# Kernel tuning notes

Hardware: AMD Instinct MI355X
Metric: run time of the kernel (lower is better)

The kernel has to match this reference:

```python
import jax, jax.numpy as jnp
import numpy as np

N = 100000   # nodes
E = 1600000  # edges
IN, HID, OUT = 128, 128, 64

def setup_inputs() -> dict:
    key = jax.random.key(0)
    ks = jax.random.split(key, 18)
    def lin(k, i, o):
        kw, kb = jax.random.split(k)
        s = 1.0 / np.sqrt(i)
        return (jax.random.uniform(kw, (i, o), jnp.float32, -s, s),
                jax.random.uniform(kb, (o,), jnp.float32, -s, s))
    x = jax.random.normal(ks[0], (N, IN), jnp.float32)
    edge_index = jax.random.randint(ks[1], (2, E), 0, N, jnp.int64)
    W1, b1   = lin(ks[2], IN, HID)
    W21, b21 = lin(ks[3], IN, HID)
    W22, b22 = lin(ks[4], HID, HID)
    W31, b31 = lin(ks[5], IN, HID)
    W32, b32 = lin(ks[6], HID, HID)
    W33, b33 = lin(ks[7], HID, HID)
    Wa, ba   = lin(ks[8], HID, 1)
    Wf, bf   = lin(ks[9], HID, OUT)
    return dict(x=x, edge_index=edge_index, W1=W1, b1=b1, W21=W21, b21=b21,
                W22=W22, b22=b22, W31=W31, b31=b31, W32=W32, b32=b32,
                W33=W33, b33=b33, Wa=Wa, ba=ba, Wf=Wf, bf=bf)

def _gcn(x, W, b, src, dst, dinv):
    # PyG GCNConv: D^{-1/2}(A+I)D^{-1/2} X W + b, self-loops added.
    h = x @ W                                    # [N, F]
    norm = dinv[src] * dinv[dst]                 # [E]
    agg = jax.ops.segment_sum(h[src] * norm[:, None], dst, num_segments=N)
    agg = agg + h * (dinv * dinv)[:, None]       # self-loop contribution
    return agg + b

def reference(x, edge_index, W1, b1, W21, b21, W22, b22, W31, b31,
              W32, b32, W33, b33, Wa, ba, Wf, bf):
    src, dst = edge_index[0], edge_index[1]
    # degree with self-loops (in-degree at target nodes)
    deg = jax.ops.segment_sum(jnp.ones(E, x.dtype), dst, num_segments=N) + 1.0
    dinv = jax.lax.rsqrt(deg)
    h1 = jax.nn.relu(_gcn(x, W1, b1, src, dst, dinv))
    h2 = jax.nn.relu(_gcn(x, W21, b21, src, dst, dinv))
    h2 = jax.nn.relu(_gcn(h2, W22, b22, src, dst, dinv))
    h3 = jax.nn.relu(_gcn(x, W31, b31, src, dst, dinv))
    h3 = jax.nn.relu(_gcn(h3, W32, b32, src, dst, dinv))
    h3 = jax.nn.relu(_gcn(h3, W33, b33, src, dst, dinv))
    H = jnp.stack([h1, h2, h3], axis=1)          # [N, 3, HID]
    scores = H @ Wa + ba                         # [N, 3, 1]
    w = jax.nn.softmax(scores, axis=1)
    h_meta = jnp.sum(w * H, axis=1)              # [N, HID]
    h_out = h_meta + h1
    return h_out @ Wf + bf                       # [N, OUT]
```

## Files before the change

kernel.cpp:

```cpp
#include <hip/hip_runtime.h>
#include <hip/hip_bf16.h>

#define HIDF 128
#define OUTF 64
#define SCAN_B 256

__device__ __forceinline__ float us2f(unsigned u_lo16) {
    return __uint_as_float(u_lo16 << 16);
}
__device__ __forceinline__ unsigned short f2us(float f) {
    __hip_bfloat16 h = __float2bfloat16(f);
    return *reinterpret_cast<unsigned short*>(&h);
}
__device__ __forceinline__ unsigned pack2(float a, float b) {
    return (unsigned)f2us(a) | ((unsigned)f2us(b) << 16);
}

__global__ __launch_bounds__(256) void deg_zero(int* __restrict__ d, int N) {
    int i = blockIdx.x * 256 + threadIdx.x;
    if (i < N) d[i] = 0;
}

__global__ __launch_bounds__(256) void deg_count(const int* __restrict__ ei, int* __restrict__ d, int E) {
    int e = blockIdx.x * 256 + threadIdx.x;
    if (e < E) atomicAdd(&d[ei[E + e]], 1);
}

__global__ __launch_bounds__(256) void scanA(const int* __restrict__ degi, int* __restrict__ blocksum, int N) {
    __shared__ int red[256];
    const int b = blockIdx.x;
    const int chunk = (N + SCAN_B - 1) / SCAN_B;
    const int lo = b * chunk, hi = min(lo + chunk, N);
    int s = 0;
    for (int i = lo + threadIdx.x; i < hi; i += 256) s += degi[i];
    red[threadIdx.x] = s;
    __syncthreads();
    for (int off = 128; off; off >>= 1) {
        if (threadIdx.x < off) red[threadIdx.x] += red[threadIdx.x + off];
        __syncthreads();
    }
    if (threadIdx.x == 0) blocksum[b] = red[0];
}

__global__ __launch_bounds__(256) void scanB(const int* __restrict__ blocksum, int* __restrict__ blockoff) {
    __shared__ int ps[256];
    const int t = threadIdx.x;
    ps[t] = blocksum[t];
    __syncthreads();
    for (int off = 1; off < 256; off <<= 1) {
        int v = ps[t];
        int u = (t >= off) ? ps[t - off] : 0;
        __syncthreads();
        ps[t] = v + u;
        __syncthreads();
    }
    blockoff[t] = (t == 0) ? 0 : ps[t - 1];
}

__global__ __launch_bounds__(256) void scanC(const int* __restrict__ degi,
                                             const int* __restrict__ blockoff,
                                             int* __restrict__ cursor,
                                             float* __restrict__ dinv, int N) {
    __shared__ int ps[256];
    const int b = blockIdx.x;
    const int chunk = (N + SCAN_B - 1) / SCAN_B;
    const int lo = b * chunk, hi = min(lo + chunk, N);
    const int tchunk = (chunk + 255) / 256;
    const int tlo = lo + threadIdx.x * tchunk;
    const int thi = min(tlo + tchunk, hi);
    int s = 0;
    for (int i = tlo; i < thi; ++i) s += degi[i];
    ps[threadIdx.x] = s;
    __syncthreads();
    for (int off = 1; off < 256; off <<= 1) {
        int v = ps[threadIdx.x];
        int u = (threadIdx.x >= off) ? ps[threadIdx.x - off] : 0;
        __syncthreads();
        ps[threadIdx.x] = v + u;
        __syncthreads();
    }
    int base = blockoff[b] + ((threadIdx.x == 0) ? 0 : ps[threadIdx.x - 1]);
    for (int i = tlo; i < thi; ++i) {
        int d = degi[i];
        cursor[i] = base;
        base += d;
        dinv[i] = rsqrtf((float)d + 1.f);
    }
}

__global__ __launch_bounds__(256) void scatter_kernel(const int* __restrict__ ei,
                                                      int* __restrict__ cursor,
                                                      int* __restrict__ csr_src, int E) {
    int e = blockIdx.x * 256 + threadIdx.x;
    if (e >= E) return;
    int pos = atomicAdd(&cursor[ei[E + e]], 1);
    csr_src[pos] = ei[e];
}

__global__ __launch_bounds__(256) void cvt_scale(const float* __restrict__ X,
                                                 const float* __restrict__ dinv,
                                                 unsigned short* __restrict__ TB, int N) {
    int g = blockIdx.x * 256 + threadIdx.x;
    if (g >= N * 32) return;
    int n = g >> 5;
    float dv = dinv[n];
    float4 v = ((const float4*)X)[g];
    ushort4 o;
    o.x = f2us(v.x * dv); o.y = f2us(v.y * dv);
    o.z = f2us(v.z * dv); o.w = f2us(v.w * dv);
    ((ushort4*)TB)[g] = o;
}

template <bool OUT_BF16>
__global__ __launch_bounds__(256) void agg_b(const unsigned short* __restrict__ TB,
                                             const float* __restrict__ dinv,
                                             const int* __restrict__ csr_src,
                                             const int* __restrict__ rend,
                                             void* __restrict__ O, int N) {
    const int n = (blockIdx.x * 256 + threadIdx.x) >> 6;
    const int lane = threadIdx.x & 63;
    if (n >= N) return;
    const int start = (n == 0) ? 0 : rend[n - 1];
    const int end   = rend[n];
    const unsigned* Tv = (const unsigned*)TB;

    float ax0 = 0.f, ay0 = 0.f, ax1 = 0.f, ay1 = 0.f;
    int e = start;
    for (; e + 8 <= end; e += 8) {
        int s0 = csr_src[e + 0], s1 = csr_src[e + 1], s2 = csr_src[e + 2], s3 = csr_src[e + 3];
        int s4 = csr_src[e + 4], s5 = csr_src[e + 5], s6 = csr_src[e + 6], s7 = csr_src[e + 7];
        unsigned v0 = Tv[(size_t)s0 * 64 + lane];
        unsigned v1 = Tv[(size_t)s1 * 64 + lane];
        unsigned v2 = Tv[(size_t)s2 * 64 + lane];
        unsigned v3 = Tv[(size_t)s3 * 64 + lane];
        unsigned v4 = Tv[(size_t)s4 * 64 + lane];
        unsigned v5 = Tv[(size_t)s5 * 64 + lane];
        unsigned v6 = Tv[(size_t)s6 * 64 + lane];
        unsigned v7 = Tv[(size_t)s7 * 64 + lane];
        ax0 += us2f(v0 & 0xffffu); ay0 += __uint_as_float(v0 & 0xffff0000u);
        ax1 += us2f(v1 & 0xffffu); ay1 += __uint_as_float(v1 & 0xffff0000u);
        ax0 += us2f(v2 & 0xffffu); ay0 += __uint_as_float(v2 & 0xffff0000u);
        ax1 += us2f(v3 & 0xffffu); ay1 += __uint_as_float(v3 & 0xffff0000u);
        ax0 += us2f(v4 & 0xffffu); ay0 += __uint_as_float(v4 & 0xffff0000u);
        ax1 += us2f(v5 & 0xffffu); ay1 += __uint_as_float(v5 & 0xffff0000u);
        ax0 += us2f(v6 & 0xffffu); ay0 += __uint_as_float(v6 & 0xffff0000u);
        ax1 += us2f(v7 & 0xffffu); ay1 += __uint_as_float(v7 & 0xffff0000u);
    }
    if (e + 4 <= end) {
        int s0 = csr_src[e + 0], s1 = csr_src[e + 1], s2 = csr_src[e + 2], s3 = csr_src[e + 3];
        unsigned v0 = Tv[(size_t)s0 * 64 + lane];
        unsigned v1 = Tv[(size_t)s1 * 64 + lane];
        unsigned v2 = Tv[(size_t)s2 * 64 + lane];
        unsigned v3 = Tv[(size_t)s3 * 64 + lane];
        ax0 += us2f(v0 & 0xffffu); ay0 += __uint_as_float(v0 & 0xffff0000u);
        ax1 += us2f(v1 & 0xffffu); ay1 += __uint_as_float(v1 & 0xffff0000u);
        ax0 += us2f(v2 & 0xffffu); ay0 += __uint_as_float(v2 & 0xffff0000u);
        ax1 += us2f(v3 & 0xffffu); ay1 += __uint_as_float(v3 & 0xffff0000u);
        e += 4;
    }
    for (; e < end; ++e) {
        int s = csr_src[e];
        unsigned v = Tv[(size_t)s * 64 + lane];
        ax0 += us2f(v & 0xffffu);
        ay0 += __uint_as_float(v & 0xffff0000u);
    }
    unsigned sv = Tv[(size_t)n * 64 + lane];
    ax0 += us2f(sv & 0xffffu);
    ay0 += __uint_as_float(sv & 0xffff0000u);
    const float dv = dinv[n];
    float ox = (ax0 + ax1) * dv;
    float oy = (ay0 + ay1) * dv;
    if (OUT_BF16) {
        ((unsigned*)O)[(size_t)n * 64 + lane] = pack2(ox, oy);
    } else {
        float2 o; o.x = ox; o.y = oy;
        ((float2*)O)[(size_t)n * 64 + lane] = o;
    }
}

__global__ __launch_bounds__(256) void agg_dual(const unsigned short* __restrict__ TB23,
                                                const float* __restrict__ dinv,
                                                const int* __restrict__ csr_src,
                                                const int* __restrict__ rend,
                                                unsigned* __restrict__ OA,
                                                unsigned* __restrict__ OB, int N) {
    const int n = (blockIdx.x * 256 + threadIdx.x) >> 6;
    const int lane = threadIdx.x & 63;
    if (n >= N) return;
    const int start = (n == 0) ? 0 : rend[n - 1];
    const int end   = rend[n];
    const unsigned* Tv = (const unsigned*)TB23;

    float ax2 = 0.f, ay2 = 0.f, bx2 = 0.f, by2 = 0.f;
    float ax3 = 0.f, ay3 = 0.f, bx3 = 0.f, by3 = 0.f;
    int e = start;
    for (; e + 4 <= end; e += 4) {
        int s0 = csr_src[e + 0], s1 = csr_src[e + 1], s2 = csr_src[e + 2], s3 = csr_src[e + 3];
        unsigned a0 = Tv[(size_t)s0 * 128 + lane];
        unsigned c0 = Tv[(size_t)s0 * 128 + 64 + lane];
        unsigned a1 = Tv[(size_t)s1 * 128 + lane];
        unsigned c1 = Tv[(size_t)s1 * 128 + 64 + lane];
        unsigned a2 = Tv[(size_t)s2 * 128 + lane];
        unsigned c2 = Tv[(size_t)s2 * 128 + 64 + lane];
        unsigned a3 = Tv[(size_t)s3 * 128 + lane];
        unsigned c3 = Tv[(size_t)s3 * 128 + 64 + lane];
        ax2 += us2f(a0 & 0xffffu); ay2 += __uint_as_float(a0 & 0xffff0000u);
        ax3 += us2f(c0 & 0xffffu); ay3 += __uint_as_float(c0 & 0xffff0000u);
        bx2 += us2f(a1 & 0xffffu); by2 += __uint_as_float(a1 & 0xffff0000u);
        bx3 += us2f(c1 & 0xffffu); by3 += __uint_as_float(c1 & 0xffff0000u);
        ax2 += us2f(a2 & 0xffffu); ay2 += __uint_as_float(a2 & 0xffff0000u);
        ax3 += us2f(c2 & 0xffffu); ay3 += __uint_as_float(c2 & 0xffff0000u);
        bx2 += us2f(a3 & 0xffffu); by2 += __uint_as_float(a3 & 0xffff0000u);
        bx3 += us2f(c3 & 0xffffu); by3 += __uint_as_float(c3 & 0xffff0000u);
    }
    for (; e < end; ++e) {
        int s = csr_src[e];
        unsigned a = Tv[(size_t)s * 128 + lane];
        unsigned c = Tv[(size_t)s * 128 + 64 + lane];
        ax2 += us2f(a & 0xffffu); ay2 += __uint_as_float(a & 0xffff0000u);
        ax3 += us2f(c & 0xffffu); ay3 += __uint_as_float(c & 0xffff0000u);
    }
    {
        unsigned a = Tv[(size_t)n * 128 + lane];
        unsigned c = Tv[(size_t)n * 128 + 64 + lane];
        ax2 += us2f(a & 0xffffu); ay2 += __uint_as_float(a & 0xffff0000u);
        ax3 += us2f(c & 0xffffu); ay3 += __uint_as_float(c & 0xffff0000u);
    }
    const float dv = dinv[n];
    OA[(size_t)n * 64 + lane] = pack2((ax2 + bx2) * dv, (ay2 + by2) * dv);
    OB[(size_t)n * 64 + lane] = pack2((ax3 + bx3) * dv, (ay3 + by3) * dv);
}

#define IM_F32 0
#define IM_BF16 1
#define OM_F32 0
#define OM_BF16 1
#define OM_BF16_SR 2
template <int IMODE, int OMODE>
__global__ __launch_bounds__(256) void gemm128d(const void* __restrict__ Xv,
                                                const float* __restrict__ W,
                                                const float* __restrict__ bias,
                                                const float* __restrict__ dinv,
                                                void* __restrict__ T, int N) {
    __shared__ float Xs[HIDF][68];
    const int tid = threadIdx.x;
    const int nb = blockIdx.x * 64;

    {
        const int nloc = tid & 63;
        const int n = nb + nloc;
        const int kq0 = tid >> 6;
        if (n < N) {
            if (IMODE == IM_F32) {
                const float4* Xr = (const float4*)((const float*)Xv + (size_t)n * HIDF);
                #pragma unroll
                for (int kq = kq0; kq < 32; kq += 4) {
                    float4 v = Xr[kq];
                    int k = kq * 4;
                    Xs[k + 0][nloc] = v.x;
                    Xs[k + 1][nloc] = v.y;
                    Xs[k + 2][nloc] = v.z;
                    Xs[k + 3][nloc] = v.w;
                }
            } else {
                const ushort4* Xr = (const ushort4*)((const unsigned short*)Xv + (size_t)n * HIDF);
                #pragma unroll
                for (int kq = kq0; kq < 32; kq += 4) {
                    ushort4 v = Xr[kq];
                    int k = kq * 4;
                    Xs[k + 0][nloc] = us2f(v.x);
                    Xs[k + 1][nloc] = us2f(v.y);
                    Xs[k + 2][nloc] = us2f(v.z);
                    Xs[k + 3][nloc] = us2f(v.w);
                }
            }
        } else {
            #pragma unroll
            for (int kq = kq0; kq < 32; kq += 4) {
                int k = kq * 4;
                Xs[k + 0][nloc] = 0.f; Xs[k + 1][nloc] = 0.f;
                Xs[k + 2][nloc] = 0.f; Xs[k + 3][nloc] = 0.f;
            }
        }
    }
    __syncthreads();

    const int j4  = tid & 31;
    const int sub = tid >> 5;
    const float4* Wrow = (const float4*)W;
    const float4 bv = ((const float4*)bias)[j4];

    float4 acc[8];
    #pragma unroll
    for (int i = 0; i < 8; ++i) acc[i] = bv;

    #pragma unroll 4
    for (int k = 0; k < HIDF; ++k) {
        float4 w = Wrow[k * 32 + j4];
        float xv[8];
        *(float4*)&xv[0] = *(const float4*)&Xs[k][sub * 8];
        *(float4*)&xv[4] = *(const float4*)&Xs[k][sub * 8 + 4];
        #pragma unroll
        for (int i = 0; i < 8; ++i) {
            acc[i].x = fmaf(xv[i], w.x, acc[i].x);
            acc[i].y = fmaf(xv[i], w.y, acc[i].y);
            acc[i].z = fmaf(xv[i], w.z, acc[i].z);
            acc[i].w = fmaf(xv[i], w.w, acc[i].w);
        }
    }

    #pragma unroll
    for (int i = 0; i < 8; ++i) {
        int n = nb + sub * 8 + i;
        if (n >= N) continue;
        float4 o = acc[i];
        if (OMODE == OM_BF16_SR) {
            float dv = dinv[n];
            o.x = fmaxf(o.x, 0.f) * dv; o.y = fmaxf(o.y, 0.f) * dv;
            o.z = fmaxf(o.z, 0.f) * dv; o.w = fmaxf(o.w, 0.f) * dv;
        }
        if (OMODE == OM_F32) {
            *((float4*)((float*)T + (size_t)n * HIDF + j4 * 4)) = o;
        } else {
            ushort4 u;
            u.x = f2us(o.x); u.y = f2us(o.y); u.z = f2us(o.z); u.w = f2us(o.w);
            *((ushort4*)((unsigned short*)T + (size_t)n * HIDF + j4 * 4)) = u;
        }
    }
}

__global__ __launch_bounds__(256) void gemm_dualA(const float* __restrict__ X,
                                                  const float* __restrict__ W21,
                                                  const float* __restrict__ b21,
                                                  const float* __restrict__ W31,
                                                  const float* __restrict__ b31,
                                                  const float* __restrict__ dinv,
                                                  unsigned short* __restrict__ TB23, int N) {
    __shared__ float Xs[HIDF][68];
    const int tid = threadIdx.x;
    const int nb = blockIdx.x * 64;

    {
        const int nloc = tid & 63;
        const int n = nb + nloc;
        const int kq0 = tid >> 6;
        if (n < N) {
            const float4* Xr = (const float4*)(X + (size_t)n * HIDF);
            #pragma unroll
            for (int kq = kq0; kq < 32; kq += 4) {
                float4 v = Xr[kq];
                int k = kq * 4;
                Xs[k + 0][nloc] = v.x;
                Xs[k + 1][nloc] = v.y;
                Xs[k + 2][nloc] = v.z;
                Xs[k + 3][nloc] = v.w;
            }
        } else {
            #pragma unroll
            for (int kq = kq0; kq < 32; kq += 4) {
                int k = kq * 4;
                Xs[k + 0][nloc] = 0.f; Xs[k + 1][nloc] = 0.f;
                Xs[k + 2][nloc] = 0.f; Xs[k + 3][nloc] = 0.f;
            }
        }
    }
    __syncthreads();

    const int j4  = tid & 31;
    const int sub = tid >> 5;
    const float4* W2r = (const float4*)W21;
    const float4* W3r = (const float4*)W31;
    const float4 bv2 = ((const float4*)b21)[j4];
    const float4 bv3 = ((const float4*)b31)[j4];

    float4 acc2[8], acc3[8];
    #pragma unroll
    for (int i = 0; i < 8; ++i) { acc2[i] = bv2; acc3[i] = bv3; }

    #pragma unroll 2
    for (int k = 0; k < HIDF; ++k) {
        float4 w2 = W2r[k * 32 + j4];
        float4 w3 = W3r[k * 32 + j4];
        float xv[8];
        *(float4*)&xv[0] = *(const float4*)&Xs[k][sub * 8];
        *(float4*)&xv[4] = *(const float4*)&Xs[k][sub * 8 + 4];
        #pragma unroll
        for (int i = 0; i < 8; ++i) {
            acc2[i].x = fmaf(xv[i], w2.x, acc2[i].x);
            acc2[i].y = fmaf(xv[i], w2.y, acc2[i].y);
            acc2[i].z = fmaf(xv[i], w2.z, acc2[i].z);
            acc2[i].w = fmaf(xv[i], w2.w, acc2[i].w);
            acc3[i].x = fmaf(xv[i], w3.x, acc3[i].x);
            acc3[i].y = fmaf(xv[i], w3.y, acc3[i].y);
            acc3[i].z = fmaf(xv[i], w3.z, acc3[i].z);
            acc3[i].w = fmaf(xv[i], w3.w, acc3[i].w);
        }
    }

    #pragma unroll
    for (int i = 0; i < 8; ++i) {
        int n = nb + sub * 8 + i;
        if (n >= N) continue;
        float dv = dinv[n];
        float4 o2 = acc2[i], o3 = acc3[i];
        ushort4 u2, u3;
        u2.x = f2us(fmaxf(o2.x, 0.f) * dv); u2.y = f2us(fmaxf(o2.y, 0.f) * dv);
        u2.z = f2us(fmaxf(o2.z, 0.f) * dv); u2.w = f2us(fmaxf(o2.w, 0.f) * dv);
        u3.x = f2us(fmaxf(o3.x, 0.f) * dv); u3.y = f2us(fmaxf(o3.y, 0.f) * dv);
        u3.z = f2us(fmaxf(o3.z, 0.f) * dv); u3.w = f2us(fmaxf(o3.w, 0.f) * dv);
        unsigned short* base = TB23 + (size_t)n * 256;
        *((ushort4*)(base + j4 * 4)) = u2;
        *((ushort4*)(base + 128 + j4 * 4)) = u3;
    }
}

__global__ __launch_bounds__(256) void meta_kernel(const float* __restrict__ H1,
                                                   const unsigned short* __restrict__ H2B,
                                                   const unsigned short* __restrict__ H3B,
                                                   const float* __restrict__ Wa,
                                                   const float* __restrict__ ba,
                                                   const float* __restrict__ Wf,
                                                   const float* __restrict__ bfb,
                                                   float* __restrict__ out, int N) {
    __shared__ float WfS[HIDF * OUTF];
    __shared__ float WaS[HIDF];
    __shared__ float hm[4][HIDF];
    const int tid = threadIdx.x;
    for (int i = tid; i < HIDF * OUTF; i += 256) WfS[i] = Wf[i];
    if (tid < HIDF) WaS[tid] = Wa[tid];
    __syncthreads();
    const float bav = ba[0];
    const int w = tid >> 6;
    const int l = tid & 63;
    const float bfv = bfb[l];
    const int iters = (N + 3) >> 2;

    for (int it = blockIdx.x; it < iters; it += gridDim.x) {
        const int n = it * 4 + w;
        __syncthreads();
        if (n < N) {
            const float* h1 = H1 + (size_t)n * HIDF;
            const unsigned short* h2 = H2B + (size_t)n * HIDF;
            const unsigned short* h3 = H3B + (size_t)n * HIDF;
            float h1a = fmaxf(h1[l], 0.f),            h1b = fmaxf(h1[l + 64], 0.f);
            float h2a = fmaxf(us2f(h2[l]), 0.f),      h2b = fmaxf(us2f(h2[l + 64]), 0.f);
            float h3a = fmaxf(us2f(h3[l]), 0.f),      h3b = fmaxf(us2f(h3[l + 64]), 0.f);
            float s1 = h1a * WaS[l] + h1b * WaS[l + 64];
            float s2 = h2a * WaS[l] + h2b * WaS[l + 64];
            float s3 = h3a * WaS[l] + h3b * WaS[l + 64];
            #pragma unroll
            for (int off = 32; off; off >>= 1) {
                s1 += __shfl_xor(s1, off);
                s2 += __shfl_xor(s2, off);
                s3 += __shfl_xor(s3, off);
            }
            s1 += bav; s2 += bav; s3 += bav;
            float m  = fmaxf(s1, fmaxf(s2, s3));
            float e1 = expf(s1 - m), e2 = expf(s2 - m), e3 = expf(s3 - m);
            float inv = 1.f / (e1 + e2 + e3);
            float w1 = e1 * inv, w2 = e2 * inv, w3 = e3 * inv;
            hm[w][l]      = w1 * h1a + w2 * h2a + w3 * h3a + h1a;
            hm[w][l + 64] = w1 * h1b + w2 * h2b + w3 * h3b + h1b;
        }
        __syncthreads();
        if (n < N) {
            float acc = bfv;
            #pragma unroll
            for (int k = 0; k < HIDF; ++k) acc = fmaf(hm[w][k], WfS[k * OUTF + l], acc);
            out[(size_t)n * OUTF + l] = acc;
        }
    }
}

extern "C" void kernel_launch(void* const* d_in, const int* in_sizes, int n_in,
                              void* d_out, int out_size, void* d_ws, size_t ws_size,
                              hipStream_t stream) {
    const float* x   = (const float*)d_in[0];
    const int*   ei  = (const int*)d_in[1];
    const float *W1  = (const float*)d_in[2],  *b1  = (const float*)d_in[3];
    const float *W21 = (const float*)d_in[4],  *b21 = (const float*)d_in[5];
    const float *W22 = (const float*)d_in[6],  *b22 = (const float*)d_in[7];
    const float *W31 = (const float*)d_in[8],  *b31 = (const float*)d_in[9];
    const float *W32 = (const float*)d_in[10], *b32 = (const float*)d_in[11];
    const float *W33 = (const float*)d_in[12], *b33 = (const float*)d_in[13];
    const float *Wa  = (const float*)d_in[14], *ba  = (const float*)d_in[15];
    const float *Wf  = (const float*)d_in[16], *bfb = (const float*)d_in[17];

    const int N = in_sizes[0] / HIDF;
    const int E = in_sizes[1] / 2;

    int*   DEGI    = (int*)d_ws;
    int*   CURSOR  = DEGI + N;
    int*   CSR_SRC = CURSOR + N;
    int*   BSUM    = CSR_SRC + E;
    int*   BOFF    = BSUM + 256;
    float* DINV    = (float*)(BOFF + 256);
    unsigned short* TB23 = (unsigned short*)(DINV + N);
    float* PX      = (float*)(TB23 + (size_t)N * 256);
    unsigned* AGA  = (unsigned*)(PX + (size_t)N * HIDF);
    unsigned* AGB  = AGA + (size_t)N * 64;
    unsigned* H2B  = AGB + (size_t)N * 64;

    const int gN    = (N + 255) / 256;
    const int gE    = (E + 255) / 256;
    const int gCVT  = (N * 32 + 255) / 256;
    const int gAGG  = (N * 64 + 255) / 256;
    const int gGEMM = (N + 63) / 64;
    const int gMETA = 2048;

    deg_zero<<<gN, 256, 0, stream>>>(DEGI, N);
    deg_count<<<gE, 256, 0, stream>>>(ei, DEGI, E);
    scanA<<<SCAN_B, 256, 0, stream>>>(DEGI, BSUM, N);
    scanB<<<1, 256, 0, stream>>>(BSUM, BOFF);
    scanC<<<SCAN_B, 256, 0, stream>>>(DEGI, BOFF, CURSOR, DINV, N);
    scatter_kernel<<<gE, 256, 0, stream>>>(ei, CURSOR, CSR_SRC, E);

    unsigned short* TBX = TB23;

    cvt_scale<<<gCVT, 256, 0, stream>>>(x, DINV, TBX, N);
    agg_b<false><<<gAGG, 256, 0, stream>>>(TBX, DINV, CSR_SRC, CURSOR, PX, N);

    gemm_dualA<<<gGEMM, 256, 0, stream>>>(PX, W21, b21, W31, b31, DINV, TB23, N);
    agg_dual<<<gAGG, 256, 0, stream>>>(TB23, DINV, CSR_SRC, CURSOR, AGA, AGB, N);

    gemm128d<IM_BF16, OM_BF16><<<gGEMM, 256, 0, stream>>>(AGA, W22, b22, DINV, H2B, N);
    gemm128d<IM_BF16, OM_BF16_SR><<<gGEMM, 256, 0, stream>>>(AGB, W32, b32, DINV, TBX, N);
    agg_b<true><<<gAGG, 256, 0, stream>>>(TBX, DINV, CSR_SRC, CURSOR, AGA, N);
    gemm128d<IM_BF16, OM_BF16><<<gGEMM, 256, 0, stream>>>(AGA, W33, b33, DINV, AGB, N);

    gemm128d<IM_F32, OM_F32><<<gGEMM, 256, 0, stream>>>(PX, W1, b1, DINV, PX, N);

    meta_kernel<<<gMETA, 256, 0, stream>>>(PX, (const unsigned short*)H2B,
                                           (const unsigned short*)AGB, Wa, ba, Wf, bfb,
                                           (float*)d_out, N);
}
```

Before: 853.6 us.

## Move hidden-layer GEMMs to bf16 MFMA with pre-transposed swizzled weights

Replaces the fp32 FMA GEMM kernels for W21, W31, W22, W32 and W33 with a bf16 MFMA 16x16x32 kernel that stages swizzled X and transposed W tiles in shared memory. A new kernel converts and transposes the five weight matrices to bf16 once per call. The fused dual GEMM is split into two MFMA launches that write interleaved halves, so PX is read twice. This trades fp32 weight and input precision for matrix-core throughput, and the scalar 2-byte output stores may be less efficient than the earlier vector stores.

```diff
diff --git a/kernel.cpp b/kernel.cpp
--- a/kernel.cpp
+++ b/kernel.cpp
@@ -4,6 +4,9 @@
 #define HIDF 128
 #define OUTF 64
 #define SCAN_B 256
+
+typedef __attribute__((ext_vector_type(8))) short bf16x8;
+typedef __attribute__((ext_vector_type(4))) float f32x4;
 
 __device__ __forceinline__ float us2f(unsigned u_lo16) {
     return __uint_as_float(u_lo16 << 16);
@@ -109,6 +112,20 @@
     o.x = f2us(v.x * dv); o.y = f2us(v.y * dv);
     o.z = f2us(v.z * dv); o.w = f2us(v.w * dv);
     ((ushort4*)TB)[g] = o;
+}
+
+__global__ __launch_bounds__(256) void cvt_w(const float* __restrict__ Wa0,
+                                             const float* __restrict__ Wa1,
+                                             const float* __restrict__ Wa2,
+                                             const float* __restrict__ Wa3,
+                                             const float* __restrict__ Wa4,
+                                             unsigned short* __restrict__ WTB) {
+    int t = blockIdx.x * 256 + threadIdx.x;
+    if (t >= 5 * 16384) return;
+    int m = t >> 14, local = t & 16383;
+    int n = local >> 7, k = local & 127;
+    const float* src = (m == 0) ? Wa0 : (m == 1) ? Wa1 : (m == 2) ? Wa2 : (m == 3) ? Wa3 : Wa4;
+    WTB[t] = f2us(src[k * 128 + n]);
 }
 
 template <bool OUT_BF16>
@@ -231,115 +248,102 @@
     OB[(size_t)n * 64 + lane] = pack2((ax3 + bx3) * dv, (ay3 + by3) * dv);
 }
 
-#define IM_F32 0
-#define IM_BF16 1
-#define OM_F32 0
 #define OM_BF16 1
 #define OM_BF16_SR 2
-template <int IMODE, int OMODE>
-__global__ __launch_bounds__(256) void gemm128d(const void* __restrict__ Xv,
+template <int OMODE, int OSTRIDE, bool INF32>
+__global__ __launch_bounds__(256) void gemm_mfma(const void* __restrict__ Xv,
+                                                 const unsigned short* __restrict__ WT,
+                                                 const float* __restrict__ bias,
+                                                 const float* __restrict__ dinv,
+                                                 unsigned short* __restrict__ T, int N) {
+    __shared__ unsigned short Xs[64 * 128];
+    __shared__ unsigned short Ws[128 * 128];
+    const int tid = threadIdx.x;
+    const int nb = blockIdx.x * 64;
+
+    for (int c = tid; c < 2048; c += 256) {
+        int n = c >> 4, kc = c & 15;
+        ((uint4*)Ws)[(n << 4) | (kc ^ (n & 7))] = ((const uint4*)WT)[c];
+    }
+    for (int c = tid; c < 1024; c += 256) {
+        int nl = c >> 4, kc = c & 15;
+        int n = nb + nl;
+        uint4 v = make_uint4(0u, 0u, 0u, 0u);
+        if (n < N) {
+            if (INF32) {
+                const float4* Xr = (const float4*)((const float*)Xv + (size_t)n * HIDF);
+                float4 v0 = Xr[kc * 2], v1 = Xr[kc * 2 + 1];
+                v.x = pack2(v0.x, v0.y); v.y = pack2(v0.z, v0.w);
+                v.z = pack2(v1.x, v1.y); v.w = pack2(v1.z, v1.w);
+            } else {
+                v = ((const uint4*)((const unsigned short*)Xv + (size_t)n * HIDF))[kc];
+            }
+        }
+        ((uint4*)Xs)[(nl << 4) | (kc ^ (nl & 7))] = v;
+    }
+    __syncthreads();
+
+    const int wv   = tid >> 6;
+    const int l    = tid & 63;
+    const int row  = l & 15;
+    const int kgrp = l >> 4;
+
+    bf16x8 afr[4];
+    #pragma unroll
+    for (int kk = 0; kk < 4; ++kk) {
+        int nl = 16 * wv + row;
+        int kc = kk * 4 + kgrp;
+        afr[kk] = *(const bf16x8*)(Xs + nl * 128 + ((kc ^ (nl & 7)) << 3));
+    }
+
+    f32x4 acc[8];
+    #pragma unroll
+    for (int nt = 0; nt < 8; ++nt) {
+        float b = bias[nt * 16 + row];
+        acc[nt] = (f32x4){b, b, b, b};
+    }
+
+    #pragma unroll
+    for (int nt = 0; nt < 8; ++nt) {
+        int col = nt * 16 + row;
+        #pragma unroll
+        for (int kk = 0; kk < 4; ++kk) {
+            int kc = kk * 4 + kgrp;
+            bf16x8 bfr = *(const bf16x8*)(Ws + col * 128 + ((kc ^ (col & 7)) << 3));
+            acc[nt] = __builtin_amdgcn_mfma_f32_16x16x32_bf16(afr[kk], bfr, acc[nt], 0, 0, 0);
+        }
+    }
+
+    float dv[4];
+    if (OMODE == OM_BF16_SR) {
+        #pragma unroll
+        for (int r = 0; r < 4; ++r) {
+            int grow = nb + 16 * wv + kgrp * 4 + r;
+            dv[r] = (grow < N) ? dinv[grow] : 0.f;
+        }
+    }
+    #pragma unroll
+    for (int nt = 0; nt < 8; ++nt) {
+        int gcol = nt * 16 + row;
+        #pragma unroll
+        for (int r = 0; r < 4; ++r) {
+            int grow = nb + 16 * wv + kgrp * 4 + r;
+            if (grow < N) {
+                float v = acc[nt][r];
+                if (OMODE == OM_BF16_SR) v = fmaxf(v, 0.f) * dv[r];
+                T[(size_t)grow * OSTRIDE + gcol] = f2us(v);
+            }
+        }
+    }
+}
+
+__global__ __launch_bounds__(256) void gemm128f(const float* __restrict__ X,
                                                 const float* __restrict__ W,
                                                 const float* __restrict__ bias,
-                                                const float* __restrict__ dinv,
-                                                void* __restrict__ T, int N) {
-    __shared__ float Xs[HIDF][68];
+                                                float* __restrict__ T, int N) {
+    __shared__ float Xsh[HIDF][68];
     const int tid = threadIdx.x;
     const int nb = blockIdx.x * 64;
-
-    {
-        const int nloc = tid & 63;
-        const int n = nb + nloc;
-        const int kq0 = tid >> 6;
-        if (n < N) {
-            if (IMODE == IM_F32) {
-                const float4* Xr = (const float4*)((const float*)Xv + (size_t)n * HIDF);
-                #pragma unroll
-                for (int kq = kq0; kq < 32; kq += 4) {
-                    float4 v = Xr[kq];
-                    int k = kq * 4;
-                    Xs[k + 0][nloc] = v.x;
-                    Xs[k + 1][nloc] = v.y;
-                    Xs[k + 2][nloc] = v.z;
-                    Xs[k + 3][nloc] = v.w;
-                }
-            } else {
-                const ushort4* Xr = (const ushort4*)((const unsigned short*)Xv + (size_t)n * HIDF);
-                #pragma unroll
-                for (int kq = kq0; kq < 32; kq += 4) {
-                    ushort4 v = Xr[kq];
-                    int k = kq * 4;
-                    Xs[k + 0][nloc] = us2f(v.x);
-                    Xs[k + 1][nloc] = us2f(v.y);
-                    Xs[k + 2][nloc] = us2f(v.z);
-                    Xs[k + 3][nloc] = us2f(v.w);
-                }
-            }
-        } else {
-            #pragma unroll
-            for (int kq = kq0; kq < 32; kq += 4) {
-                int k = kq * 4;
-                Xs[k + 0][nloc] = 0.f; Xs[k + 1][nloc] = 0.f;
-                Xs[k + 2][nloc] = 0.f; Xs[k + 3][nloc] = 0.f;
-            }
-        }
-    }
-    __syncthreads();
-
-    const int j4  = tid & 31;
-    const int sub = tid >> 5;
-    const float4* Wrow = (const float4*)W;
-    const float4 bv = ((const float4*)bias)[j4];
-
-    float4 acc[8];
-    #pragma unroll
-    for (int i = 0; i < 8; ++i) acc[i] = bv;
-
-    #pragma unroll 4
-    for (int k = 0; k < HIDF; ++k) {
-        float4 w = Wrow[k * 32 + j4];
-        float xv[8];
-        *(float4*)&xv[0] = *(const float4*)&Xs[k][sub * 8];
-        *(float4*)&xv[4] = *(const float4*)&Xs[k][sub * 8 + 4];
-        #pragma unroll
-        for (int i = 0; i < 8; ++i) {
-            acc[i].x = fmaf(xv[i], w.x, acc[i].x);
-            acc[i].y = fmaf(xv[i], w.y, acc[i].y);
-            acc[i].z = fmaf(xv[i], w.z, acc[i].z);
-            acc[i].w = fmaf(xv[i], w.w, acc[i].w);
-        }
-    }
-
-    #pragma unroll
-    for (int i = 0; i < 8; ++i) {
-        int n = nb + sub * 8 + i;
-        if (n >= N) continue;
-        float4 o = acc[i];
-        if (OMODE == OM_BF16_SR) {
-            float dv = dinv[n];
-            o.x = fmaxf(o.x, 0.f) * dv; o.y = fmaxf(o.y, 0.f) * dv;
-            o.z = fmaxf(o.z, 0.f) * dv; o.w = fmaxf(o.w, 0.f) * dv;
-        }
-        if (OMODE == OM_F32) {
-            *((float4*)((float*)T + (size_t)n * HIDF + j4 * 4)) = o;
-        } else {
-            ushort4 u;
-            u.x = f2us(o.x); u.y = f2us(o.y); u.z = f2us(o.z); u.w = f2us(o.w);
-            *((ushort4*)((unsigned short*)T + (size_t)n * HIDF + j4 * 4)) = u;
-        }
-    }
-}
-
-__global__ __launch_bounds__(256) void gemm_dualA(const float* __restrict__ X,
-                                                  const float* __restrict__ W21,
-                                                  const float* __restrict__ b21,
-                                                  const float* __restrict__ W31,
-                                                  const float* __restrict__ b31,
-                                                  const float* __restrict__ dinv,
-                                                  unsigned short* __restrict__ TB23, int N) {
-    __shared__ float Xs[HIDF][68];
-    const int tid = threadIdx.x;
-    const int nb = blockIdx.x * 64;
-
     {
         const int nloc = tid & 63;
         const int n = nb + nloc;
@@ -350,17 +354,15 @@
             for (int kq = kq0; kq < 32; kq += 4) {
                 float4 v = Xr[kq];
                 int k = kq * 4;
-                Xs[k + 0][nloc] = v.x;
-                Xs[k + 1][nloc] = v.y;
-                Xs[k + 2][nloc] = v.z;
-                Xs[k + 3][nloc] = v.w;
+                Xsh[k + 0][nloc] = v.x; Xsh[k + 1][nloc] = v.y;
+                Xsh[k + 2][nloc] = v.z; Xsh[k + 3][nloc] = v.w;
             }
         } else {
             #pragma unroll
             for (int kq = kq0; kq < 32; kq += 4) {
                 int k = kq * 4;
-                Xs[k + 0][nloc] = 0.f; Xs[k + 1][nloc] = 0.f;
-                Xs[k + 2][nloc] = 0.f; Xs[k + 3][nloc] = 0.f;
+                Xsh[k + 0][nloc] = 0.f; Xsh[k + 1][nloc] = 0.f;
+                Xsh[k + 2][nloc] = 0.f; Xsh[k + 3][nloc] = 0.f;
             }
         }
     }
@@ -368,49 +370,31 @@
 
     const int j4  = tid & 31;
     const int sub = tid >> 5;
-    const float4* W2r = (const float4*)W21;
-    const float4* W3r = (const float4*)W31;
-    const float4 bv2 = ((const float4*)b21)[j4];
-    const float4 bv3 = ((const float4*)b31)[j4];
-
-    float4 acc2[8], acc3[8];
+    const float4* Wrow = (const float4*)W;
+    const float4 bv = ((const float4*)bias)[j4];
+
+    float4 acc[8];
     #pragma unroll
-    for (int i = 0; i < 8; ++i) { acc2[i] = bv2; acc3[i] = bv3; }
-
-    #pragma unroll 2
+    for (int i = 0; i < 8; ++i) acc[i] = bv;
+
+    #pragma unroll 4
     for (int k = 0; k < HIDF; ++k) {
-        float4 w2 = W2r[k * 32 + j4];
-        float4 w3 = W3r[k * 32 + j4];
+        float4 w = Wrow[k * 32 + j4];
         float xv[8];
-        *(float4*)&xv[0] = *(const float4*)&Xs[k][sub * 8];
-        *(float4*)&xv[4] = *(const float4*)&Xs[k][sub * 8 + 4];
+        *(float4*)&xv[0] = *(const float4*)&Xsh[k][sub * 8];
+        *(float4*)&xv[4] = *(const float4*)&Xsh[k][sub * 8 + 4];
         #pragma unroll
         for (int i = 0; i < 8; ++i) {
-            acc2[i].x = fmaf(xv[i], w2.x, acc2[i].x);
-            acc2[i].y = fmaf(xv[i], w2.y, acc2[i].y);
-            acc2[i].z = fmaf(xv[i], w2.z, acc2[i].z);
-            acc2[i].w = fmaf(xv[i], w2.w, acc2[i].w);
-            acc3[i].x = fmaf(xv[i], w3.x, acc3[i].x);
-            acc3[i].y = fmaf(xv[i], w3.y, acc3[i].y);
-            acc3[i].z = fmaf(xv[i], w3.z, acc3[i].z);
-            acc3[i].w = fmaf(xv[i], w3.w, acc3[i].w);
-        }
-    }
-
+            acc[i].x = fmaf(xv[i], w.x, acc[i].x);
+            acc[i].y = fmaf(xv[i], w.y, acc[i].y);
+            acc[i].z = fmaf(xv[i], w.z, acc[i].z);
+            acc[i].w = fmaf(xv[i], w.w, acc[i].w);
+        }
+    }
     #pragma unroll
     for (int i = 0; i < 8; ++i) {
         int n = nb + sub * 8 + i;
-        if (n >= N) continue;
-        float dv = dinv[n];
-        float4 o2 = acc2[i], o3 = acc3[i];
-        ushort4 u2, u3;
-        u2.x = f2us(fmaxf(o2.x, 0.f) * dv); u2.y = f2us(fmaxf(o2.y, 0.f) * dv);
-        u2.z = f2us(fmaxf(o2.z, 0.f) * dv); u2.w = f2us(fmaxf(o2.w, 0.f) * dv);
-        u3.x = f2us(fmaxf(o3.x, 0.f) * dv); u3.y = f2us(fmaxf(o3.y, 0.f) * dv);
-        u3.z = f2us(fmaxf(o3.z, 0.f) * dv); u3.w = f2us(fmaxf(o3.w, 0.f) * dv);
-        unsigned short* base = TB23 + (size_t)n * 256;
-        *((ushort4*)(base + j4 * 4)) = u2;
-        *((ushort4*)(base + 128 + j4 * 4)) = u3;
+        if (n < N) *((float4*)&T[(size_t)n * HIDF + j4 * 4]) = acc[i];
     }
 }
 
@@ -442,9 +426,9 @@
             const float* h1 = H1 + (size_t)n * HIDF;
             const unsigned short* h2 = H2B + (size_t)n * HIDF;
             const unsigned short* h3 = H3B + (size_t)n * HIDF;
-            float h1a = fmaxf(h1[l], 0.f),            h1b = fmaxf(h1[l + 64], 0.f);
-            float h2a = fmaxf(us2f(h2[l]), 0.f),      h2b = fmaxf(us2f(h2[l + 64]), 0.f);
-            float h3a = fmaxf(us2f(h3[l]), 0.f),      h3b = fmaxf(us2f(h3[l + 64]), 0.f);
+            float h1a = fmaxf(h1[l], 0.f),       h1b = fmaxf(h1[l + 64], 0.f);
+            float h2a = fmaxf(us2f(h2[l]), 0.f), h2b = fmaxf(us2f(h2[l + 64]), 0.f);
+            float h3a = fmaxf(us2f(h3[l]), 0.f), h3b = fmaxf(us2f(h3[l + 64]), 0.f);
             float s1 = h1a * WaS[l] + h1b * WaS[l + 64];
             float s2 = h2a * WaS[l] + h2b * WaS[l + 64];
             float s3 = h3a * WaS[l] + h3b * WaS[l + 64];
@@ -500,6 +484,7 @@
     unsigned* AGA  = (unsigned*)(PX + (size_t)N * HIDF);
     unsigned* AGB  = AGA + (size_t)N * 64;
     unsigned* H2B  = AGB + (size_t)N * 64;
+    unsigned short* WTB = (unsigned short*)(H2B + (size_t)N * 64);
 
     const int gN    = (N + 255) / 256;
     const int gE    = (E + 255) / 256;
@@ -514,21 +499,23 @@
     scanB<<<1, 256, 0, stream>>>(BSUM, BOFF);
     scanC<<<SCAN_B, 256, 0, stream>>>(DEGI, BOFF, CURSOR, DINV, N);
     scatter_kernel<<<gE, 256, 0, stream>>>(ei, CURSOR, CSR_SRC, E);
+    cvt_w<<<320, 256, 0, stream>>>(W21, W31, W22, W32, W33, WTB);
 
     unsigned short* TBX = TB23;
 
     cvt_scale<<<gCVT, 256, 0, stream>>>(x, DINV, TBX, N);
     agg_b<false><<<gAGG, 256, 0, stream>>>(TBX, DINV, CSR_SRC, CURSOR, PX, N);
 
-    gemm_dualA<<<gGEMM, 256, 0, stream>>>(PX, W21, b21, W31, b31, DINV, TB23, N);
+    gemm_mfma<OM_BF16_SR, 256, true><<<gGEMM, 256, 0, stream>>>(PX, WTB,           b21, DINV, TB23,       N);
+    gemm_mfma<OM_BF16_SR, 256, true><<<gGEMM, 256, 0, stream>>>(PX, WTB + 16384,   b31, DINV, TB23 + 128, N);
     agg_dual<<<gAGG, 256, 0, stream>>>(TB23, DINV, CSR_SRC, CURSOR, AGA, AGB, N);
 
-    gemm128d<IM_BF16, OM_BF16><<<gGEMM, 256, 0, stream>>>(AGA, W22, b22, DINV, H2B, N);
-    gemm128d<IM_BF16, OM_BF16_SR><<<gGEMM, 256, 0, stream>>>(AGB, W32, b32, DINV, TBX, N);
+    gemm_mfma<OM_BF16, 128, false><<<gGEMM, 256, 0, stream>>>(AGA, WTB + 2 * 16384, b22, DINV, (unsigned short*)H2B, N);
+    gemm_mfma<OM_BF16_SR, 128, false><<<gGEMM, 256, 0, stream>>>(AGB, WTB + 3 * 16384, b32, DINV, TBX, N);
     agg_b<true><<<gAGG, 256, 0, stream>>>(TBX, DINV, CSR_SRC, CURSOR, AGA, N);
-    gemm128d<IM_BF16, OM_BF16><<<gGEMM, 256, 0, stream>>>(AGA, W33, b33, DINV, AGB, N);
-
-    gemm128d<IM_F32, OM_F32><<<gGEMM, 256, 0, stream>>>(PX, W1, b1, DINV, PX, N);
+    gemm_mfma<OM_BF16, 128, false><<<gGEMM, 256, 0, stream>>>(AGA, WTB + 4 * 16384, b33, DINV, (unsigned short*)AGB, N);
+
+    gemm128f<<<gGEMM, 256, 0, stream>>>(PX, W1, b1, PX, N);
 
     meta_kernel<<<gMETA, 256, 0, stream>>>(PX, (const unsigned short*)H2B,
                                            (const unsigned short*)AGB, Wa, ba, Wf, bfb,
```

New measurement: 752.5 us. 11.8% less time.
